# Performance work log

Measured on AMD Instinct MI355X. Metric: run time of the kernel, lower is better.

The kernel has to match this reference:

```python
import jax, jax.numpy as jnp
import numpy as np

EPS = 1e-6
NUM_GROUPS = 16


def group_norm(x, gamma, beta):
    # x: [B, C, H, W]
    B, C, H, W = x.shape
    xg = x.reshape(B, NUM_GROUPS, C // NUM_GROUPS, H, W)
    mean = xg.mean(axis=(2, 3, 4), keepdims=True)
    var = xg.var(axis=(2, 3, 4), keepdims=True)
    xg = (xg - mean) * jax.lax.rsqrt(var + EPS)
    x = xg.reshape(B, C, H, W)
    return x * gamma[None, :, None, None] + beta[None, :, None, None]


def conv1x1(x, w, b):
    # x: [B, C, H, W], w: [O, C], b: [O]
    return jnp.einsum('bchw,oc->bohw', x, w) + b[None, :, None, None]


def setup_inputs() -> dict:
    key = jax.random.key(0)
    ks = jax.random.split(key, 6)
    B, C, H, W = 8, 256, 64, 64
    s = 1.0 / np.sqrt(C)
    return {
        'x': jax.random.normal(ks[0], (B, C, H, W), dtype=jnp.float32),
        'gamma': jnp.ones((C,), jnp.float32),
        'beta': jnp.zeros((C,), jnp.float32),
        'wq': jax.random.normal(ks[1], (C, C), dtype=jnp.float32) * s,
        'bq': jnp.zeros((C,), jnp.float32),
        'wk': jax.random.normal(ks[2], (C, C), dtype=jnp.float32) * s,
        'bk': jnp.zeros((C,), jnp.float32),
        'wv': jax.random.normal(ks[3], (C, C), dtype=jnp.float32) * s,
        'bv': jnp.zeros((C,), jnp.float32),
        'wp': jax.random.normal(ks[4], (C, C), dtype=jnp.float32) * s,
        'bp': jnp.zeros((C,), jnp.float32),
    }


def reference(x, gamma, beta, wq, bq, wk, bk, wv, bv, wp, bp):
    B, C, H, W = x.shape
    identity = x
    h = group_norm(x, gamma, beta)
    q = conv1x1(h, wq, bq).reshape(B, C, H * W)  # [B, C, N]
    k = conv1x1(h, wk, bk).reshape(B, C, H * W)
    v = conv1x1(h, wv, bv).reshape(B, C, H * W)
    # alpha[b, i, j] = sum_c q[b, c, i] * k[b, c, j], scaled by C^-0.5
    alpha = jnp.einsum('bci,bcj->bij', q, k) * (C ** -0.5)
    alpha = jax.nn.softmax(alpha, axis=-1)
    # out[b, c, i] = sum_j v[b, c, j] * alpha[b, i, j]
    out = jnp.einsum('bcj,bij->bci', v, alpha).reshape(B, C, H, W)
    out = conv1x1(out, wp, bp)
    return identity + out
```

## Files before the change

kernel.cpp:

```cpp
#include <hip/hip_runtime.h>
#include <hip/hip_bf16.h>


typedef unsigned int u32;
typedef unsigned short u16;
typedef __bf16 bf16x8 __attribute__((ext_vector_type(8)));
typedef float f32x4 __attribute__((ext_vector_type(4)));
typedef float f32x16 __attribute__((ext_vector_type(16)));

#define GAS __attribute__((address_space(1)))
#define LAS __attribute__((address_space(3)))

__device__ __forceinline__ u16 f2bf(float f) {
  union { float f; u32 u; } v; v.f = f;
  return (u16)((v.u + 0x7fffu + ((v.u >> 16) & 1u)) >> 16);
}

__device__ __forceinline__ f32x4 mfma16(bf16x8 a, bf16x8 b, f32x4 c) {
  return __builtin_amdgcn_mfma_f32_16x16x32_bf16(a, b, c, 0, 0, 0);
}
__device__ __forceinline__ f32x16 mfma32(bf16x8 a, bf16x8 b, f32x16 c) {
  return __builtin_amdgcn_mfma_f32_32x32x16_bf16(a, b, c, 0, 0, 0);
}

template<int ROWB, int MASK, int ITERS, int NT>
__device__ __forceinline__ void stage_swz(u16* lds, const u16* g, int ldg, int tid) {
#pragma unroll
  for (int it = 0; it < ITERS; ++it) {
    int idx = it * NT + tid;
    int off = idx * 16;
    int row = off / ROWB;
    int slot = off % ROWB;
    int sem = slot ^ ((row & MASK) << 4);
    const u16* src = g + (long)row * ldg + (sem >> 1);
    u16* dst = lds + (long)(idx & ~63) * 8;
    __builtin_amdgcn_global_load_lds((const GAS u32*)src, (LAS u32*)dst, 16, 0, 0);
  }
}

template<int ITERS, int NT>
__device__ __forceinline__ void stage_lin(u16* lds, const u16* g, int tid) {
#pragma unroll
  for (int it = 0; it < ITERS; ++it) {
    int idx = it * NT + tid;
    const u16* src = g + (long)idx * 8;
    u16* dst = lds + (long)(idx & ~63) * 8;
    __builtin_amdgcn_global_load_lds((const GAS u32*)src, (LAS u32*)dst, 16, 0, 0);
  }
}

template<int ROWB, int MASK>
__device__ __forceinline__ bf16x8 ldfrag(const u16* lds, int row, int kbyte) {
  int off = row * ROWB + (kbyte ^ ((row & MASK) << 4));
  return *(const bf16x8*)((const char*)lds + off);
}

__global__ __launch_bounds__(256) void convert_w(
    const float* __restrict__ w0, const float* __restrict__ w1,
    const float* __restrict__ w2, const float* __restrict__ w3,
    u16* __restrict__ out) {
  int i = blockIdx.x * 256 + threadIdx.x;
  int seg = i >> 16, idx = i & 65535;
  const float* w = seg == 0 ? w0 : seg == 1 ? w1 : seg == 2 ? w2 : w3;
  out[i] = f2bf(w[idx]);
}

__global__ __launch_bounds__(256) void gn_kernel(
    const float* __restrict__ x, const float* __restrict__ gamma,
    const float* __restrict__ beta, u16* __restrict__ ht) {
  int tid = threadIdx.x;
  int b = blockIdx.x >> 4;
  int grp = blockIdx.x & 15;
  const float* xg = x + ((long)b * 256 + grp * 16) * 4096;

  float s = 0.f, ss = 0.f;
  const float4* x4 = (const float4*)xg;
#pragma unroll 4
  for (int it = 0; it < 64; ++it) {
    float4 v = x4[it * 256 + tid];
    s += v.x + v.y + v.z + v.w;
    ss += v.x * v.x + v.y * v.y + v.z * v.z + v.w * v.w;
  }
#pragma unroll
  for (int d = 1; d < 64; d <<= 1) {
    s += __shfl_xor(s, d);
    ss += __shfl_xor(ss, d);
  }
  __shared__ float red[10];
  int lane = tid & 63, wave = tid >> 6;
  if (lane == 0) { red[wave] = s; red[4 + wave] = ss; }
  __syncthreads();
  if (tid == 0) {
    float S = red[0] + red[1] + red[2] + red[3];
    float SS = red[4] + red[5] + red[6] + red[7];
    float mean = S * (1.f / 65536.f);
    float var = SS * (1.f / 65536.f) - mean * mean;
    red[8] = mean;
    red[9] = rsqrtf(var + 1e-6f);
  }
  __syncthreads();
  float mean = red[8], rstd = red[9];

  float a[16], bb[16];
#pragma unroll
  for (int c = 0; c < 16; ++c) {
    float gm = gamma[grp * 16 + c];
    float bt = beta[grp * 16 + c];
    a[c] = gm * rstd;
    bb[c] = bt - mean * a[c];
  }
  u16* hb = ht + (long)b * 4096 * 256 + grp * 16;
  for (int it = 0; it < 16; ++it) {
    int n = it * 256 + tid;
    __align__(16) u16 tmp[16];
#pragma unroll
    for (int c = 0; c < 16; ++c)
      tmp[c] = f2bf(xg[(long)c * 4096 + n] * a[c] + bb[c]);
    u16* dst = hb + (long)n * 256;
    ((uint4*)dst)[0] = ((uint4*)tmp)[0];
    ((uint4*)dst)[1] = ((uint4*)tmp)[1];
  }
}

__global__ __launch_bounds__(256) void gemm_qkv(
    const u16* __restrict__ ht, const u16* __restrict__ wbf,
    u16* __restrict__ qtb, u16* __restrict__ ktb, u16* __restrict__ vcb,
    const float* __restrict__ bq, const float* __restrict__ bk,
    const float* __restrict__ bv) {
  __shared__ __align__(16) u16 as[64 * 64];
  __shared__ __align__(16) u16 bqs[64 * 64];
  __shared__ __align__(16) u16 bks[64 * 64];
  __shared__ __align__(16) u16 bvs[64 * 64];
  int tid = threadIdx.x;
  int lane = tid & 63, wave = tid >> 6;
  int g = lane >> 4, lr = lane & 15;
  int wm = wave >> 1, wn = wave & 1;
  const u16* Ab = ht + (long)blockIdx.x * 64 * 256;
  const u16* Wq = wbf + (long)blockIdx.y * 64 * 256;

  f32x4 zero = {0.f, 0.f, 0.f, 0.f};
  f32x4 acc[3][2][2];
#pragma unroll
  for (int w = 0; w < 3; ++w)
#pragma unroll
    for (int i = 0; i < 2; ++i)
#pragma unroll
      for (int j = 0; j < 2; ++j) acc[w][i][j] = zero;

  for (int k0 = 0; k0 < 256; k0 += 64) {
    stage_swz<128, 7, 2, 256>(as, Ab + k0, 256, tid);
    stage_swz<128, 7, 2, 256>(bqs, Wq + k0, 256, tid);
    stage_swz<128, 7, 2, 256>(bks, Wq + 65536 + k0, 256, tid);
    stage_swz<128, 7, 2, 256>(bvs, Wq + 131072 + k0, 256, tid);
    __syncthreads();
#pragma unroll
    for (int ks = 0; ks < 2; ++ks) {
      int kb = ks * 64 + g * 16;
      bf16x8 a0 = ldfrag<128, 7>(as, wm * 32 + lr, kb);
      bf16x8 a1 = ldfrag<128, 7>(as, wm * 32 + 16 + lr, kb);
      __builtin_amdgcn_s_setprio(1);
      {
        bf16x8 b0 = ldfrag<128, 7>(bqs, wn * 32 + lr, kb);
        bf16x8 b1 = ldfrag<128, 7>(bqs, wn * 32 + 16 + lr, kb);
        acc[0][0][0] = mfma16(a0, b0, acc[0][0][0]);
        acc[0][0][1] = mfma16(a0, b1, acc[0][0][1]);
        acc[0][1][0] = mfma16(a1, b0, acc[0][1][0]);
        acc[0][1][1] = mfma16(a1, b1, acc[0][1][1]);
      }
      {
        bf16x8 b0 = ldfrag<128, 7>(bks, wn * 32 + lr, kb);
        bf16x8 b1 = ldfrag<128, 7>(bks, wn * 32 + 16 + lr, kb);
        acc[1][0][0] = mfma16(a0, b0, acc[1][0][0]);
        acc[1][0][1] = mfma16(a0, b1, acc[1][0][1]);
        acc[1][1][0] = mfma16(a1, b0, acc[1][1][0]);
        acc[1][1][1] = mfma16(a1, b1, acc[1][1][1]);
      }
      {
        bf16x8 b0 = ldfrag<128, 7>(bvs, wn * 32 + lr, kb);
        bf16x8 b1 = ldfrag<128, 7>(bvs, wn * 32 + 16 + lr, kb);
        acc[2][0][0] = mfma16(a0, b0, acc[2][0][0]);
        acc[2][0][1] = mfma16(a0, b1, acc[2][0][1]);
        acc[2][1][0] = mfma16(a1, b0, acc[2][1][0]);
        acc[2][1][1] = mfma16(a1, b1, acc[2][1][1]);
      }
      __builtin_amdgcn_s_setprio(0);
    }
    __syncthreads();
  }

  const float QSC = 0.0625f * 1.44269504f;
  int mb = blockIdx.x * 64 + wm * 32;
  int nb = blockIdx.y * 64 + wn * 32;
  int b_ = mb >> 12;
  int posb = mb & 4095;
#pragma unroll
  for (int mi = 0; mi < 2; ++mi)
#pragma unroll
    for (int ni = 0; ni < 2; ++ni) {
      int n = nb + ni * 16 + lr;
      int pos0 = posb + mi * 16 + 4 * g;
      int jt = pos0 >> 5, jj = pos0 & 31;
      long kbase = (long)b_ * 1048576 + (long)jt * 8192 + (n >> 3) * 256 + jj * 8 + (n & 7);
      __align__(8) u16 v4[4];
#pragma unroll
      for (int e = 0; e < 4; ++e) {
        int m = mb + mi * 16 + 4 * g + e;
        long addr = (long)m * 256 + n;
        qtb[addr] = f2bf((acc[0][mi][ni][e] + bq[n]) * QSC);
        ktb[kbase + e * 8] = f2bf(acc[1][mi][ni][e] + bk[n]);
        v4[e] = f2bf(acc[2][mi][ni][e] + bv[n]);
      }
      int gg = (pos0 >> 3) & 3, js = pos0 & 7;
      *(uint2*)(vcb + (long)b_ * 1048576 + (long)jt * 8192 + gg * 2048 + n * 8 + js)
          = *(uint2*)v4;
    }
}

__global__ __launch_bounds__(256) void gemm_proj(
    const u16* __restrict__ A, const u16* __restrict__ Bt,
    float* __restrict__ outp, const float* __restrict__ bias,
    const float* __restrict__ resid) {
  __shared__ __align__(16) u16 as[64 * 64];
  __shared__ __align__(16) u16 bs[64 * 64];
  int tid = threadIdx.x;
  int lane = tid & 63, wave = tid >> 6;
  int g = lane >> 4, lr = lane & 15;
  int wm = wave >> 1, wn = wave & 1;
  int z = blockIdx.z;
  const u16* Ab = A + (long)blockIdx.x * 64 * 256;
  const u16* Bb = Bt + (long)z * 4096 * 256 + (long)blockIdx.y * 64 * 256;

  f32x4 zero = {0.f, 0.f, 0.f, 0.f};
  f32x4 acc[2][2];
#pragma unroll
  for (int i = 0; i < 2; ++i)
#pragma unroll
    for (int j = 0; j < 2; ++j) acc[i][j] = zero;

  for (int k0 = 0; k0 < 256; k0 += 64) {
    stage_swz<128, 7, 2, 256>(as, Ab + k0, 256, tid);
    stage_swz<128, 7, 2, 256>(bs, Bb + k0, 256, tid);
    __syncthreads();
#pragma unroll
    for (int ks = 0; ks < 2; ++ks) {
      int kb = ks * 64 + g * 16;
      bf16x8 a0 = ldfrag<128, 7>(as, wm * 32 + lr, kb);
      bf16x8 a1 = ldfrag<128, 7>(as, wm * 32 + 16 + lr, kb);
      bf16x8 b0 = ldfrag<128, 7>(bs, wn * 32 + lr, kb);
      bf16x8 b1 = ldfrag<128, 7>(bs, wn * 32 + 16 + lr, kb);
      acc[0][0] = mfma16(a0, b0, acc[0][0]);
      acc[0][1] = mfma16(a0, b1, acc[0][1]);
      acc[1][0] = mfma16(a1, b0, acc[1][0]);
      acc[1][1] = mfma16(a1, b1, acc[1][1]);
    }
    __syncthreads();
  }

  int mb = blockIdx.x * 64 + wm * 32;
  int nb = blockIdx.y * 64 + wn * 32;
#pragma unroll
  for (int mi = 0; mi < 2; ++mi)
#pragma unroll
    for (int ni = 0; ni < 2; ++ni)
#pragma unroll
      for (int e = 0; e < 4; ++e) {
        int m = mb + mi * 16 + 4 * g + e;
        int n = nb + ni * 16 + lr;
        long addr = (long)z * 1048576 + (long)m * 4096 + n;
        outp[addr] = acc[mi][ni][e] + bias[m] + resid[addr];
      }
}

__global__ __launch_bounds__(128, 2) void attn_flash(
    const u16* __restrict__ qt, const u16* __restrict__ kgp,
    const u16* __restrict__ vgp, u16* __restrict__ part0, u16* __restrict__ part1,
    float2* __restrict__ ml0, float2* __restrict__ ml1) {
  __shared__ __align__(16) u16 ksT[8192];
  __shared__ __align__(16) u16 vsT[8192];
  __shared__ float fws[64];

  int tid = threadIdx.x;
  int lane = tid & 63;
  int h = lane >> 5, lr = lane & 31;
  int rg = tid >> 6;
  int bid = blockIdx.x;
  long b = bid & 7;
  int jhalf = (bid >> 3) & 1;
  int i0 = (bid >> 4) * 64;

  const u16* kb = kgp + b * 1048576 + (long)(jhalf * 64) * 8192;
  const u16* vb = vgp + b * 1048576 + (long)(jhalf * 64) * 8192;
  float* fw = fws + rg * 32;

  const u16* qrow = qt + ((b * 4096 + i0 + rg * 32 + lr) << 8) + h * 8;
  bf16x8 qreg[16];
#pragma unroll
  for (int kk = 0; kk < 16; ++kk)
    qreg[kk] = *(const bf16x8*)(qrow + kk * 16);

  f32x16 zero16 = {0,0,0,0,0,0,0,0,0,0,0,0,0,0,0,0};
  f32x16 acc[8];
#pragma unroll
  for (int ct = 0; ct < 8; ++ct) acc[ct] = zero16;
  float mrun = -3e38f, lsum = 0.f;

  for (int t = 0; t < 64; ++t) {
    __syncthreads();
    stage_lin<8, 128>(ksT, kb + (long)t * 8192, tid);
    stage_lin<8, 128>(vsT, vb + (long)t * 8192, tid);
    __syncthreads();

    f32x16 sacc = zero16;
    __builtin_amdgcn_s_setprio(1);
#pragma unroll
    for (int kk = 0; kk < 16; ++kk) {
      bf16x8 kf = *(const bf16x8*)(ksT + ((2 * kk + h) * 32 + lr) * 8);
      sacc = mfma32(kf, qreg[kk], sacc);
    }
    __builtin_amdgcn_s_setprio(0);

    float m0 = fmaxf(fmaxf(sacc[0], sacc[1]), fmaxf(sacc[2], sacc[3]));
    float m1 = fmaxf(fmaxf(sacc[4], sacc[5]), fmaxf(sacc[6], sacc[7]));
    float m2 = fmaxf(fmaxf(sacc[8], sacc[9]), fmaxf(sacc[10], sacc[11]));
    float m3 = fmaxf(fmaxf(sacc[12], sacc[13]), fmaxf(sacc[14], sacc[15]));
    float mloc = fmaxf(fmaxf(m0, m1), fmaxf(m2, m3));
    mloc = fmaxf(mloc, __shfl_xor(mloc, 32));

    if (!__all(mloc - mrun <= 8.f)) {
      float mnew = fmaxf(mrun, mloc);
      float al = exp2f(mrun - mnew);
      mrun = mnew;
      lsum *= al;
      if (h == 0) fw[lr] = al;
      asm volatile("s_waitcnt lgkmcnt(0)" ::: "memory");
      f32x4 fq0 = *(const f32x4*)&fw[4 * h];
      f32x4 fq1 = *(const f32x4*)&fw[8 + 4 * h];
      f32x4 fq2 = *(const f32x4*)&fw[16 + 4 * h];
      f32x4 fq3 = *(const f32x4*)&fw[24 + 4 * h];
      f32x16 alv;
#pragma unroll
      for (int e = 0; e < 4; ++e) {
        alv[e] = fq0[e]; alv[4 + e] = fq1[e]; alv[8 + e] = fq2[e]; alv[12 + e] = fq3[e];
      }
#pragma unroll
      for (int ct = 0; ct < 8; ++ct) acc[ct] *= alv;
    }

    u32 u[8];
#pragma unroll
    for (int m = 0; m < 8; ++m) {
      float p0 = exp2f(sacc[2 * m] - mrun);
      float p1 = exp2f(sacc[2 * m + 1] - mrun);
      lsum += p0 + p1;
      asm volatile("v_cvt_pk_bf16_f32 %0, %1, %2" : "=v"(u[m]) : "v"(p0), "v"(p1));
    }
    u32 rv[4];
#pragma unroll
    for (int kt2 = 0; kt2 < 2; ++kt2)
#pragma unroll
      for (int idx = 0; idx < 2; ++idx) {
        u32 send = h ? u[4 * kt2 + idx] : u[4 * kt2 + 2 + idx];
        rv[kt2 * 2 + idx] = (u32)__shfl_xor((int)send, 32);
      }
    union { u32 wd[4]; bf16x8 v; } pf[2];
#pragma unroll
    for (int kt2 = 0; kt2 < 2; ++kt2) {
      pf[kt2].wd[0] = h ? rv[kt2 * 2] : u[4 * kt2];
      pf[kt2].wd[1] = h ? rv[kt2 * 2 + 1] : u[4 * kt2 + 1];
      pf[kt2].wd[2] = h ? u[4 * kt2 + 2] : rv[kt2 * 2];
      pf[kt2].wd[3] = h ? u[4 * kt2 + 3] : rv[kt2 * 2 + 1];
    }

    __builtin_amdgcn_s_setprio(1);
#pragma unroll
    for (int ct = 0; ct < 8; ++ct) {
      int c = ct * 32 + lr;
      bf16x8 vf0 = *(const bf16x8*)(vsT + ((long)h * 256 + c) * 8);
      bf16x8 vf1 = *(const bf16x8*)(vsT + ((long)(2 + h) * 256 + c) * 8);
      acc[ct] = mfma32(pf[0].v, vf0, acc[ct]);
      acc[ct] = mfma32(pf[1].v, vf1, acc[ct]);
    }
    __builtin_amdgcn_s_setprio(0);
  }

  lsum += __shfl_xor(lsum, 32);
  u16* pout = jhalf ? part1 : part0;
  float2* mlo = jhalf ? ml1 : ml0;
  if (h == 0)
    mlo[b * 4096 + i0 + rg * 32 + lr] = make_float2(mrun, lsum);
  u16* ob = pout + ((b * 4096 + i0 + rg * 32) << 8);
#pragma unroll
  for (int ct = 0; ct < 8; ++ct) {
    int c = ct * 32 + lr;
#pragma unroll
    for (int q = 0; q < 4; ++q)
#pragma unroll
      for (int e = 0; e < 4; ++e) {
        int i = 8 * q + 4 * h + e;
        ob[(long)i * 256 + c] = f2bf(acc[ct][4 * q + e]);
      }
  }
}

__global__ __launch_bounds__(256) void attn_merge(
    const u16* __restrict__ p0, const u16* __restrict__ p1,
    const float2* __restrict__ ml0, const float2* __restrict__ ml1,
    u16* __restrict__ out) {
  int tid = threadIdx.x;
  int row = blockIdx.x * 16 + (tid >> 4);
  int cs = (tid & 15) * 16;
  float2 a = ml0[row], c = ml1[row];
  float M = fmaxf(a.x, c.x);
  float w0 = exp2f(a.x - M), w1 = exp2f(c.x - M);
  float rl = 1.0f / (w0 * a.y + w1 * c.y);
  float f0 = w0 * rl, f1 = w1 * rl;

  long base = (long)row * 256 + cs;
  bf16x8 a0 = *(const bf16x8*)(p0 + base);
  bf16x8 a1 = *(const bf16x8*)(p0 + base + 8);
  bf16x8 c0 = *(const bf16x8*)(p1 + base);
  bf16x8 c1 = *(const bf16x8*)(p1 + base + 8);
  __align__(16) u16 o[16];
#pragma unroll
  for (int k = 0; k < 8; ++k) {
    o[k]     = f2bf(f0 * (float)a0[k] + f1 * (float)c0[k]);
    o[k + 8] = f2bf(f0 * (float)a1[k] + f1 * (float)c1[k]);
  }
  *(uint4*)(out + base) = ((uint4*)o)[0];
  *(uint4*)(out + base + 8) = ((uint4*)o)[1];
}

extern "C" void kernel_launch(void* const* d_in, const int* in_sizes, int n_in,
                              void* d_out, int out_size, void* d_ws, size_t ws_size,
                              hipStream_t stream) {
  const float* x     = (const float*)d_in[0];
  const float* gamma = (const float*)d_in[1];
  const float* beta  = (const float*)d_in[2];
  const float* wq = (const float*)d_in[3];
  const float* bq = (const float*)d_in[4];
  const float* wk = (const float*)d_in[5];
  const float* bk = (const float*)d_in[6];
  const float* wv = (const float*)d_in[7];
  const float* bv = (const float*)d_in[8];
  const float* wp = (const float*)d_in[9];
  const float* bp = (const float*)d_in[10];

  char* ws = (char*)d_ws;
  const long SZ = 16777216;
  u16* ht  = (u16*)(ws);
  u16* qtb = (u16*)(ws + SZ);
  u16* ktb = (u16*)(ws + 2 * SZ);
  u16* vcb = (u16*)(ws + 3 * SZ);
  u16* wbf = (u16*)(ws + 4 * SZ);
  u16* part0 = ht;
  u16* part1 = (u16*)d_out;
  float2* ml0 = (float2*)((char*)d_out + SZ);
  float2* ml1 = (float2*)((char*)d_out + SZ + 262144);

  convert_w<<<1024, 256, 0, stream>>>(wq, wk, wv, wp, wbf);
  gn_kernel<<<128, 256, 0, stream>>>(x, gamma, beta, ht);

  dim3 gq(512, 4, 1);
  gemm_qkv<<<gq, 256, 0, stream>>>(ht, wbf, qtb, ktb, vcb, bq, bk, bv);

  attn_flash<<<1024, 128, 0, stream>>>(qtb, ktb, vcb, part0, part1, ml0, ml1);

  attn_merge<<<2048, 256, 0, stream>>>(part0, part1, ml0, ml1, qtb);

  dim3 gp(4, 64, 8);
  gemm_proj<<<gp, 256, 0, stream>>>(wbf + 3 * 65536, qtb, (float*)d_out, bp, x);
}
```

Measured before the change: 346.7 us.

## Rewrite QKV and projection GEMMs with 32x32 MFMA and larger tiles

Both 1x1-conv GEMMs now use the 32x32x16 bf16 MFMA in place of the 16x16x32 one. The QKV tile grows to 128x128 per block and the projection tile to all 256 output channels by 64 positions. The swizzled LDS staging is replaced by a k-granule-major layout (8 bf16 per row per granule) that can be read directly as MFMA fragments, with 32-wide k steps. The aim is more reuse per staged byte and fewer blocks, at the cost of fewer blocks for occupancy, unswizzled LDS reads that may conflict, and scattered epilogue stores.

Result: faster. 333.8 us (-3.7%).

```diff
diff --git a/kernel.cpp b/kernel.cpp
--- a/kernel.cpp
+++ b/kernel.cpp
@@ -16,26 +16,8 @@
   return (u16)((v.u + 0x7fffu + ((v.u >> 16) & 1u)) >> 16);
 }
 
-__device__ __forceinline__ f32x4 mfma16(bf16x8 a, bf16x8 b, f32x4 c) {
-  return __builtin_amdgcn_mfma_f32_16x16x32_bf16(a, b, c, 0, 0, 0);
-}
 __device__ __forceinline__ f32x16 mfma32(bf16x8 a, bf16x8 b, f32x16 c) {
   return __builtin_amdgcn_mfma_f32_32x32x16_bf16(a, b, c, 0, 0, 0);
-}
-
-template<int ROWB, int MASK, int ITERS, int NT>
-__device__ __forceinline__ void stage_swz(u16* lds, const u16* g, int ldg, int tid) {
-#pragma unroll
-  for (int it = 0; it < ITERS; ++it) {
-    int idx = it * NT + tid;
-    int off = idx * 16;
-    int row = off / ROWB;
-    int slot = off % ROWB;
-    int sem = slot ^ ((row & MASK) << 4);
-    const u16* src = g + (long)row * ldg + (sem >> 1);
-    u16* dst = lds + (long)(idx & ~63) * 8;
-    __builtin_amdgcn_global_load_lds((const GAS u32*)src, (LAS u32*)dst, 16, 0, 0);
-  }
 }
 
 template<int ITERS, int NT>
@@ -49,10 +31,18 @@
   }
 }
 
-template<int ROWB, int MASK>
-__device__ __forceinline__ bf16x8 ldfrag(const u16* lds, int row, int kbyte) {
-  int off = row * ROWB + (kbyte ^ ((row & MASK) << 4));
-  return *(const bf16x8*)((const char*)lds + off);
+template<int ROWS, int NT>
+__device__ __forceinline__ void stage_gran(u16* lds, const u16* g, int k0, int tid) {
+  constexpr int ITERS = 4 * ROWS / NT;
+#pragma unroll
+  for (int it = 0; it < ITERS; ++it) {
+    int gi = it * NT + tid;
+    int row = gi & (ROWS - 1);
+    int kh = gi / ROWS;
+    const u16* src = g + (long)row * 256 + k0 + kh * 8;
+    u16* dst = lds + (long)(gi & ~63) * 8;
+    __builtin_amdgcn_global_load_lds((const GAS u32*)src, (LAS u32*)dst, 16, 0, 0);
+  }
 }
 
 __global__ __launch_bounds__(256) void convert_w(
@@ -122,153 +112,155 @@
   }
 }
 
-__global__ __launch_bounds__(256) void gemm_qkv(
+__global__ __launch_bounds__(256, 2) void gemm_qkv(
     const u16* __restrict__ ht, const u16* __restrict__ wbf,
     u16* __restrict__ qtb, u16* __restrict__ ktb, u16* __restrict__ vcb,
     const float* __restrict__ bq, const float* __restrict__ bk,
     const float* __restrict__ bv) {
-  __shared__ __align__(16) u16 as[64 * 64];
-  __shared__ __align__(16) u16 bqs[64 * 64];
-  __shared__ __align__(16) u16 bks[64 * 64];
-  __shared__ __align__(16) u16 bvs[64 * 64];
+  __shared__ __align__(16) u16 as2[4 * 128 * 8];
+  __shared__ __align__(16) u16 bs2[3][4 * 128 * 8];
+
   int tid = threadIdx.x;
-  int lane = tid & 63, wave = tid >> 6;
-  int g = lane >> 4, lr = lane & 15;
-  int wm = wave >> 1, wn = wave & 1;
-  const u16* Ab = ht + (long)blockIdx.x * 64 * 256;
-  const u16* Wq = wbf + (long)blockIdx.y * 64 * 256;
-
-  f32x4 zero = {0.f, 0.f, 0.f, 0.f};
-  f32x4 acc[3][2][2];
-#pragma unroll
-  for (int w = 0; w < 3; ++w)
-#pragma unroll
-    for (int i = 0; i < 2; ++i)
-#pragma unroll
-      for (int j = 0; j < 2; ++j) acc[w][i][j] = zero;
-
-  for (int k0 = 0; k0 < 256; k0 += 64) {
-    stage_swz<128, 7, 2, 256>(as, Ab + k0, 256, tid);
-    stage_swz<128, 7, 2, 256>(bqs, Wq + k0, 256, tid);
-    stage_swz<128, 7, 2, 256>(bks, Wq + 65536 + k0, 256, tid);
-    stage_swz<128, 7, 2, 256>(bvs, Wq + 131072 + k0, 256, tid);
-    __syncthreads();
+  int lane = tid & 63;
+  int h = lane >> 5, lr = lane & 31;
+  int wave = tid >> 6;
+  int wp = wave >> 1, wo = wave & 1;
+  long mrow = (long)blockIdx.x * 128;
+  int ob = blockIdx.y * 128;
+
+  f32x16 zero16 = {0,0,0,0,0,0,0,0,0,0,0,0,0,0,0,0};
+  f32x16 acc[3][2][2];
+#pragma unroll
+  for (int m = 0; m < 3; ++m)
+#pragma unroll
+    for (int p = 0; p < 2; ++p)
+#pragma unroll
+      for (int q = 0; q < 2; ++q) acc[m][p][q] = zero16;
+
+  const u16* Ab = ht + mrow * 256;
+
+  for (int step = 0; step < 8; ++step) {
+    int k0 = step * 32;
+    __syncthreads();
+    stage_gran<128, 256>(as2, Ab, k0, tid);
+    stage_gran<128, 256>(bs2[0], wbf + (long)ob * 256, k0, tid);
+    stage_gran<128, 256>(bs2[1], wbf + 65536 + (long)ob * 256, k0, tid);
+    stage_gran<128, 256>(bs2[2], wbf + 131072 + (long)ob * 256, k0, tid);
+    __syncthreads();
+
 #pragma unroll
     for (int ks = 0; ks < 2; ++ks) {
-      int kb = ks * 64 + g * 16;
-      bf16x8 a0 = ldfrag<128, 7>(as, wm * 32 + lr, kb);
-      bf16x8 a1 = ldfrag<128, 7>(as, wm * 32 + 16 + lr, kb);
+      int kg = (2 * ks + h) * 128;
+      bf16x8 a0 = *(const bf16x8*)(as2 + (long)(kg + wp * 64 + lr) * 8);
+      bf16x8 a1 = *(const bf16x8*)(as2 + (long)(kg + wp * 64 + 32 + lr) * 8);
       __builtin_amdgcn_s_setprio(1);
-      {
-        bf16x8 b0 = ldfrag<128, 7>(bqs, wn * 32 + lr, kb);
-        bf16x8 b1 = ldfrag<128, 7>(bqs, wn * 32 + 16 + lr, kb);
-        acc[0][0][0] = mfma16(a0, b0, acc[0][0][0]);
-        acc[0][0][1] = mfma16(a0, b1, acc[0][0][1]);
-        acc[0][1][0] = mfma16(a1, b0, acc[0][1][0]);
-        acc[0][1][1] = mfma16(a1, b1, acc[0][1][1]);
-      }
-      {
-        bf16x8 b0 = ldfrag<128, 7>(bks, wn * 32 + lr, kb);
-        bf16x8 b1 = ldfrag<128, 7>(bks, wn * 32 + 16 + lr, kb);
-        acc[1][0][0] = mfma16(a0, b0, acc[1][0][0]);
-        acc[1][0][1] = mfma16(a0, b1, acc[1][0][1]);
-        acc[1][1][0] = mfma16(a1, b0, acc[1][1][0]);
-        acc[1][1][1] = mfma16(a1, b1, acc[1][1][1]);
-      }
-      {
-        bf16x8 b0 = ldfrag<128, 7>(bvs, wn * 32 + lr, kb);
-        bf16x8 b1 = ldfrag<128, 7>(bvs, wn * 32 + 16 + lr, kb);
-        acc[2][0][0] = mfma16(a0, b0, acc[2][0][0]);
-        acc[2][0][1] = mfma16(a0, b1, acc[2][0][1]);
-        acc[2][1][0] = mfma16(a1, b0, acc[2][1][0]);
-        acc[2][1][1] = mfma16(a1, b1, acc[2][1][1]);
+#pragma unroll
+      for (int m = 0; m < 3; ++m) {
+        bf16x8 b0 = *(const bf16x8*)(bs2[m] + (long)(kg + wo * 64 + lr) * 8);
+        bf16x8 b1 = *(const bf16x8*)(bs2[m] + (long)(kg + wo * 64 + 32 + lr) * 8);
+        acc[m][0][0] = mfma32(a0, b0, acc[m][0][0]);
+        acc[m][0][1] = mfma32(a0, b1, acc[m][0][1]);
+        acc[m][1][0] = mfma32(a1, b0, acc[m][1][0]);
+        acc[m][1][1] = mfma32(a1, b1, acc[m][1][1]);
       }
       __builtin_amdgcn_s_setprio(0);
     }
-    __syncthreads();
   }
 
   const float QSC = 0.0625f * 1.44269504f;
-  int mb = blockIdx.x * 64 + wm * 32;
-  int nb = blockIdx.y * 64 + wn * 32;
-  int b_ = mb >> 12;
-  int posb = mb & 4095;
-#pragma unroll
-  for (int mi = 0; mi < 2; ++mi)
-#pragma unroll
-    for (int ni = 0; ni < 2; ++ni) {
-      int n = nb + ni * 16 + lr;
-      int pos0 = posb + mi * 16 + 4 * g;
-      int jt = pos0 >> 5, jj = pos0 & 31;
-      long kbase = (long)b_ * 1048576 + (long)jt * 8192 + (n >> 3) * 256 + jj * 8 + (n & 7);
-      __align__(8) u16 v4[4];
-#pragma unroll
-      for (int e = 0; e < 4; ++e) {
-        int m = mb + mi * 16 + 4 * g + e;
-        long addr = (long)m * 256 + n;
-        qtb[addr] = f2bf((acc[0][mi][ni][e] + bq[n]) * QSC);
-        ktb[kbase + e * 8] = f2bf(acc[1][mi][ni][e] + bk[n]);
-        v4[e] = f2bf(acc[2][mi][ni][e] + bv[n]);
+  long b_ = mrow >> 12;
+  int posb = (int)(mrow & 4095);
+#pragma unroll
+  for (int p = 0; p < 2; ++p)
+#pragma unroll
+    for (int q = 0; q < 2; ++q) {
+      int o = ob + wo * 64 + q * 32 + lr;
+      float bqv = bq[o], bkv = bk[o], bvv = bv[o];
+      int posl0 = posb + wp * 64 + p * 32;
+      int jt = posl0 >> 5;
+      long tbase = b_ * 1048576 + (long)jt * 8192;
+      long kbase = tbase + (o >> 3) * 256 + (o & 7);
+      long vbase = tbase + (long)o * 8;
+      long qrow0 = (mrow + wp * 64 + p * 32) * 256 + o;
+#pragma unroll
+      for (int quad = 0; quad < 4; ++quad) {
+        __align__(8) u16 v4[4];
+#pragma unroll
+        for (int e = 0; e < 4; ++e) {
+          int rloc = 8 * quad + 4 * h + e;
+          float vq = acc[0][p][q][4 * quad + e];
+          float vk = acc[1][p][q][4 * quad + e];
+          float vv = acc[2][p][q][4 * quad + e];
+          qtb[qrow0 + (long)rloc * 256] = f2bf((vq + bqv) * QSC);
+          ktb[kbase + rloc * 8] = f2bf(vk + bkv);
+          v4[e] = f2bf(vv + bvv);
+        }
+        int r0 = 8 * quad + 4 * h;
+        *(uint2*)(vcb + vbase + ((r0 >> 3) & 3) * 2048 + (r0 & 7)) = *(uint2*)v4;
       }
-      int gg = (pos0 >> 3) & 3, js = pos0 & 7;
-      *(uint2*)(vcb + (long)b_ * 1048576 + (long)jt * 8192 + gg * 2048 + n * 8 + js)
-          = *(uint2*)v4;
     }
 }
 
 __global__ __launch_bounds__(256) void gemm_proj(
-    const u16* __restrict__ A, const u16* __restrict__ Bt,
+    const u16* __restrict__ Wp, const u16* __restrict__ ao,
     float* __restrict__ outp, const float* __restrict__ bias,
     const float* __restrict__ resid) {
-  __shared__ __align__(16) u16 as[64 * 64];
-  __shared__ __align__(16) u16 bs[64 * 64];
+  __shared__ __align__(16) u16 ws2[4 * 256 * 8];
+  __shared__ __align__(16) u16 aos[4 * 64 * 8];
+
   int tid = threadIdx.x;
-  int lane = tid & 63, wave = tid >> 6;
-  int g = lane >> 4, lr = lane & 15;
-  int wm = wave >> 1, wn = wave & 1;
-  int z = blockIdx.z;
-  const u16* Ab = A + (long)blockIdx.x * 64 * 256;
-  const u16* Bb = Bt + (long)z * 4096 * 256 + (long)blockIdx.y * 64 * 256;
-
-  f32x4 zero = {0.f, 0.f, 0.f, 0.f};
-  f32x4 acc[2][2];
-#pragma unroll
-  for (int i = 0; i < 2; ++i)
-#pragma unroll
-    for (int j = 0; j < 2; ++j) acc[i][j] = zero;
-
-  for (int k0 = 0; k0 < 256; k0 += 64) {
-    stage_swz<128, 7, 2, 256>(as, Ab + k0, 256, tid);
-    stage_swz<128, 7, 2, 256>(bs, Bb + k0, 256, tid);
-    __syncthreads();
+  int lane = tid & 63;
+  int h = lane >> 5, lr = lane & 31;
+  int wo = tid >> 6;
+  long b = blockIdx.x & 7;
+  int pos0 = (blockIdx.x >> 3) * 64;
+  const u16* aob = ao + (b * 4096 + pos0) * 256;
+
+  f32x16 zero16 = {0,0,0,0,0,0,0,0,0,0,0,0,0,0,0,0};
+  f32x16 acc[2][2];
+#pragma unroll
+  for (int p = 0; p < 2; ++p)
+#pragma unroll
+    for (int q = 0; q < 2; ++q) acc[p][q] = zero16;
+
+  for (int step = 0; step < 8; ++step) {
+    int k0 = step * 32;
+    __syncthreads();
+    stage_gran<256, 256>(ws2, Wp, k0, tid);
+    stage_gran<64, 256>(aos, aob, k0, tid);
+    __syncthreads();
+
 #pragma unroll
     for (int ks = 0; ks < 2; ++ks) {
-      int kb = ks * 64 + g * 16;
-      bf16x8 a0 = ldfrag<128, 7>(as, wm * 32 + lr, kb);
-      bf16x8 a1 = ldfrag<128, 7>(as, wm * 32 + 16 + lr, kb);
-      bf16x8 b0 = ldfrag<128, 7>(bs, wn * 32 + lr, kb);
-      bf16x8 b1 = ldfrag<128, 7>(bs, wn * 32 + 16 + lr, kb);
-      acc[0][0] = mfma16(a0, b0, acc[0][0]);
-      acc[0][1] = mfma16(a0, b1, acc[0][1]);
-      acc[1][0] = mfma16(a1, b0, acc[1][0]);
-      acc[1][1] = mfma16(a1, b1, acc[1][1]);
-    }
-    __syncthreads();
-  }
-
-  int mb = blockIdx.x * 64 + wm * 32;
-  int nb = blockIdx.y * 64 + wn * 32;
-#pragma unroll
-  for (int mi = 0; mi < 2; ++mi)
-#pragma unroll
-    for (int ni = 0; ni < 2; ++ni)
-#pragma unroll
-      for (int e = 0; e < 4; ++e) {
-        int m = mb + mi * 16 + 4 * g + e;
-        int n = nb + ni * 16 + lr;
-        long addr = (long)z * 1048576 + (long)m * 4096 + n;
-        outp[addr] = acc[mi][ni][e] + bias[m] + resid[addr];
-      }
+      int kgw = (2 * ks + h) * 256;
+      int kga = (2 * ks + h) * 64;
+      bf16x8 w0 = *(const bf16x8*)(ws2 + (long)(kgw + wo * 64 + lr) * 8);
+      bf16x8 w1 = *(const bf16x8*)(ws2 + (long)(kgw + wo * 64 + 32 + lr) * 8);
+      bf16x8 o0 = *(const bf16x8*)(aos + (long)(kga + lr) * 8);
+      bf16x8 o1 = *(const bf16x8*)(aos + (long)(kga + 32 + lr) * 8);
+      __builtin_amdgcn_s_setprio(1);
+      acc[0][0] = mfma32(w0, o0, acc[0][0]);
+      acc[0][1] = mfma32(w0, o1, acc[0][1]);
+      acc[1][0] = mfma32(w1, o0, acc[1][0]);
+      acc[1][1] = mfma32(w1, o1, acc[1][1]);
+      __builtin_amdgcn_s_setprio(0);
+    }
+  }
+
+#pragma unroll
+  for (int p = 0; p < 2; ++p)
+#pragma unroll
+    for (int q = 0; q < 2; ++q) {
+      int pos = pos0 + q * 32 + lr;
+#pragma unroll
+      for (int quad = 0; quad < 4; ++quad)
+#pragma unroll
+        for (int e = 0; e < 4; ++e) {
+          int o = wo * 64 + p * 32 + 8 * quad + 4 * h + e;
+          long addr = b * 1048576 + (long)o * 4096 + pos;
+          outp[addr] = acc[p][q][4 * quad + e] + bias[o] + resid[addr];
+        }
+    }
 }
 
 __global__ __launch_bounds__(128, 2) void attn_flash(
@@ -460,13 +452,13 @@
   convert_w<<<1024, 256, 0, stream>>>(wq, wk, wv, wp, wbf);
   gn_kernel<<<128, 256, 0, stream>>>(x, gamma, beta, ht);
 
-  dim3 gq(512, 4, 1);
+  dim3 gq(256, 2, 1);
   gemm_qkv<<<gq, 256, 0, stream>>>(ht, wbf, qtb, ktb, vcb, bq, bk, bv);
 
   attn_flash<<<1024, 128, 0, stream>>>(qtb, ktb, vcb, part0, part1, ml0, ml1);
 
   attn_merge<<<2048, 256, 0, stream>>>(part0, part1, ml0, ml1, qtb);
 
-  dim3 gp(4, 64, 8);
+  dim3 gp(512, 1, 1);
   gemm_proj<<<gp, 256, 0, stream>>>(wbf + 3 * 65536, qtb, (float*)d_out, bp, x);
 }
```
